# Kernel tuning notes

Measured on AMD Instinct MI355X. Metric: run time of the kernel, lower is better.

Reference implementation:

```python
import jax, jax.numpy as jnp
import numpy as np

LAYER_NAMES = ["self", "cross", "self", "cross", "self", "cross"]
L = len(LAYER_NAMES)
D = 256          # feature_dim
H = 4            # num_heads
HEAD_DIM = D // H
BS = 2           # image pairs
N = 1024         # keypoints per image
BN_EPS = 1e-5


def _conv1x1(x, W, b):
    # x: [B, Cin, N], W: [Cout, Cin] -> [B, Cout, N]  (Conv1d kernel_size=1)
    return jnp.einsum('oi,bin->bon', W, x) + b[None, :, None]


def _batchnorm1d(x, gamma, beta):
    # training-mode BatchNorm1d over [B, C, N]: stats over (B, N) per channel
    mean = jnp.mean(x, axis=(0, 2), keepdims=True)
    var = jnp.var(x, axis=(0, 2), keepdims=True)
    return (x - mean) * jax.lax.rsqrt(var + BN_EPS) * gamma[None, :, None] + beta[None, :, None]


def _attention(q_in, k_in, v_in, mask, Wq, bq, Wk, bk, Wv, bv, Wm, bm):
    B = q_in.shape[0]
    q = _conv1x1(q_in, Wq, bq).reshape(B, HEAD_DIM, H, -1)   # [B, d, h, n]
    k = _conv1x1(k_in, Wk, bk).reshape(B, HEAD_DIM, H, -1)
    v = _conv1x1(v_in, Wv, bv).reshape(B, HEAD_DIM, H, -1)
    scores = jnp.einsum('bdhn,bdhm->bhnm', q, k) / (HEAD_DIM ** 0.5)
    # multiplicative mask (NOT additive), applied before softmax
    scores = scores * mask[:, None, :, :]
    prob = jax.nn.softmax(scores, axis=-1)
    x = jnp.einsum('bhnm,bdhm->bdhn', prob, v)               # [B, d, h, n]
    return _conv1x1(x.reshape(B, D, -1), Wm, bm)             # merge


def _gnn(desc0, desc1, M0, M1, Wq, bq, Wk, bk, Wv, bv, Wm, bm, W1, b1, g1, beta1, W2, b2):
    bs = desc0.shape[0]
    mask = jnp.concatenate([M0, M1], axis=0)                 # [2bs, N, N]
    for i, name in enumerate(LAYER_NAMES):
        x = jnp.concatenate([desc0, desc1], axis=0)          # [2bs, D, N]
        src = jnp.concatenate([desc1, desc0], axis=0) if name == 'cross' else x
        message = _attention(x, src, src, mask,
                             Wq[i], bq[i], Wk[i], bk[i], Wv[i], bv[i], Wm[i], bm[i])
        y = jnp.concatenate([x, message], axis=1)            # [2bs, 2D, N]
        y = jax.nn.relu(_batchnorm1d(_conv1x1(y, W1[i], b1[i]), g1[i], beta1[i]))
        delta = _conv1x1(y, W2[i], b2[i])                    # [2bs, D, N]
        desc0 = desc0 + delta[:bs]
        desc1 = desc1 + delta[bs:]
    # concat the two updated descriptor sets along batch for a single output array
    return jnp.concatenate([desc0, desc1], axis=0)


def setup_inputs() -> dict:
    key = jax.random.key(0)
    ks = jax.random.split(key, 12)
    s = 0.02
    return {
        'desc0': jax.random.normal(ks[0], (BS, D, N), jnp.float32),
        'desc1': jax.random.normal(ks[1], (BS, D, N), jnp.float32),
        'M0': jnp.ones((BS, N, N), jnp.float32),
        'M1': jnp.ones((BS, N, N), jnp.float32),
        'Wq': jax.random.normal(ks[2], (L, D, D), jnp.float32) * s,
        'bq': jnp.zeros((L, D), jnp.float32),
        'Wk': jax.random.normal(ks[3], (L, D, D), jnp.float32) * s,
        'bk': jnp.zeros((L, D), jnp.float32),
        'Wv': jax.random.normal(ks[4], (L, D, D), jnp.float32) * s,
        'bv': jnp.zeros((L, D), jnp.float32),
        'Wm': jax.random.normal(ks[5], (L, D, D), jnp.float32) * s,
        'bm': jnp.zeros((L, D), jnp.float32),
        'W1': jax.random.normal(ks[6], (L, 2 * D, 2 * D), jnp.float32) * s,
        'b1': jnp.zeros((L, 2 * D), jnp.float32),
        'g1': jnp.ones((L, 2 * D), jnp.float32),
        'beta1': jnp.zeros((L, 2 * D), jnp.float32),
        'W2': jax.random.normal(ks[7], (L, D, 2 * D), jnp.float32) * s,
        'b2': jnp.zeros((L, D), jnp.float32),
    }


def reference(desc0, desc1, M0, M1, Wq, bq, Wk, bk, Wv, bv, Wm, bm, W1, b1, g1, beta1, W2, b2):
    return _gnn(desc0, desc1, M0, M1, Wq, bq, Wk, bk, Wv, bv, Wm, bm, W1, b1, g1, beta1, W2, b2)
```

## Files before the change

kernel.cpp:

```cpp
#include <hip/hip_runtime.h>
#include <hip/hip_bf16.h>

#define NN 1024
#define DD 256
#define LL 6

typedef __attribute__((ext_vector_type(8))) short bf16x8;
typedef __attribute__((ext_vector_type(4))) float f32x4;
typedef __attribute__((ext_vector_type(4))) unsigned short u16x4;

__device__ __forceinline__ unsigned short f2bf(float f) {
    union { float f; unsigned u; } x; x.f = f;
    return (unsigned short)((x.u + 0x7fffu + ((x.u >> 16) & 1u)) >> 16);
}

__device__ __forceinline__ unsigned short f2bf_trunc(float f) {
    union { float f; unsigned u; } x; x.f = f;
    return (unsigned short)(x.u >> 16);
}

__device__ __forceinline__ float bf2f(unsigned short u) {
    union { unsigned u; float f; } x; x.u = ((unsigned)u) << 16; return x.f;
}

__device__ __forceinline__ f32x4 mfma16(bf16x8 a, bf16x8 b, f32x4 c) {
    return __builtin_amdgcn_mfma_f32_16x16x32_bf16(a, b, c, 0, 0, 0);
}

__device__ __forceinline__ void gll16(const unsigned short* g, unsigned short* l) {
    __builtin_amdgcn_global_load_lds(
        (const __attribute__((address_space(1))) unsigned int*)g,
        (__attribute__((address_space(3))) unsigned int*)l, 16, 0, 0);
}

__global__ __launch_bounds__(256) void prep_kernel(
    const float* __restrict__ desc0, const float* __restrict__ desc1,
    const float* __restrict__ M0, const float* __restrict__ M1,
    const float* __restrict__ Wq, const float* __restrict__ Wk,
    const float* __restrict__ Wv, const float* __restrict__ Wm,
    const float* __restrict__ W1, const float* __restrict__ W2,
    const float* __restrict__ bm, const float* __restrict__ b1,
    unsigned short* __restrict__ wbf, unsigned short* __restrict__ maskbf,
    float* __restrict__ bmix, float* __restrict__ desc, unsigned short* __restrict__ xbf) {
    __shared__ float T[32][33];
    const int SQ = LL * 65536;
    const int S1 = LL * 262144;
    int blk = blockIdx.x, tid = threadIdx.x;
    if (blk < 3840) {
        int idx = blk * 256 + tid;
        size_t base = (size_t)idx * 4;
        f32x4 v;
        if (base < (size_t)4 * SQ) {
            int seg = (int)(base / SQ), off = (int)(base % SQ);
            const float* p = (seg == 0) ? Wq : (seg == 1) ? Wk : (seg == 2) ? Wv : Wm;
            if (seg < 3) {
                int l = off >> 16, rem = off & 65535;
                int op = rem >> 8, i = rem & 255;
                int src = ((op & 63) << 2) | (op >> 6);
                v = *(const f32x4*)(p + (size_t)l * 65536 + (size_t)src * 256 + i);
            } else {
                v = *(const f32x4*)(p + off);
            }
        } else if (base < (size_t)4 * SQ + S1) {
            v = *(const f32x4*)(W1 + base - 4 * SQ);
        } else {
            v = *(const f32x4*)(W2 + base - 4 * SQ - S1);
        }
        u16x4 o;
#pragma unroll
        for (int j = 0; j < 4; j++) o[j] = f2bf(v[j]);
        *(u16x4*)(wbf + base) = o;
    } else if (blk < 7936) {
        int idx = (blk - 3840) * 256 + tid;
        size_t base = (size_t)idx * 4;
        int bb = (int)(base >> 20);
        const float* src = (bb < 2) ? (M0 + base) : (M1 + base - (2ull << 20));
        f32x4 v = *(const f32x4*)src;
        u16x4 o;
#pragma unroll
        for (int j = 0; j < 4; j++) o[j] = f2bf(v[j]);
        *(u16x4*)(maskbf + base) = o;
    } else if (blk < 8704) {
        int lane = tid & 63;
        int wid = (blk - 7936) * 4 + (tid >> 6);
        int l = wid >> 9, o = wid & 511;
        const float* row = W1 + ((size_t)l * 512 + o) * 512 + 256;
        const float* bmr = bm + (size_t)l * 256;
        f32x4 r = *(const f32x4*)(row + lane * 4);
        f32x4 b4 = *(const f32x4*)(bmr + lane * 4);
        float acc = r[0] * b4[0] + r[1] * b4[1] + r[2] * b4[2] + r[3] * b4[3];
        acc += __shfl_xor(acc, 1, 64);
        acc += __shfl_xor(acc, 2, 64);
        acc += __shfl_xor(acc, 4, 64);
        acc += __shfl_xor(acc, 8, 64);
        acc += __shfl_xor(acc, 16, 64);
        acc += __shfl_xor(acc, 32, 64);
        if (lane == 0) bmix[wid] = b1[wid] + acc;
    } else {
        int task = blk - 8704;
        int bb = task >> 8, tt = task & 255;
        int n0 = (tt >> 3) * 32, c0 = (tt & 7) * 32;
        const float* src = (bb < 2) ? (desc0 + (size_t)bb * DD * NN)
                                    : (desc1 + (size_t)(bb - 2) * DD * NN);
        int i = tid >> 5, j = tid & 31;
#pragma unroll
        for (int r = 0; r < 4; r++) {
            int c = i + r * 8;
            T[c][j] = src[(size_t)(c0 + c) * NN + n0 + j];
        }
        __syncthreads();
#pragma unroll
        for (int r = 0; r < 4; r++) {
            int n = i + r * 8;
            float v = T[j][n];
            size_t di = ((size_t)bb * NN + n0 + n) * DD + c0 + j;
            desc[di] = v;
            xbf[di] = f2bf(v);
        }
    }
}

__global__ __launch_bounds__(256) void fold1_kernel(const unsigned short* __restrict__ W1bf,
                                                    const unsigned short* __restrict__ Wmbf,
                                                    unsigned short* __restrict__ W1m) {
    int l = blockIdx.z;
    int o0 = blockIdx.x * 64, i0 = blockIdx.y * 64;
    const unsigned short* A = W1bf + (size_t)l * 262144;
    const unsigned short* B = Wmbf + (size_t)l * 65536;
    __shared__ unsigned short Bt[64][264];
    int t = threadIdx.x;
#pragma unroll
    for (int r = 0; r < 8; r++) {
        int j = r * 32 + (t >> 3);
        int il = (t & 7) * 8;
        union { bf16x8 v; unsigned short u[8]; } ld;
        ld.v = *(const bf16x8*)(B + (size_t)j * 256 + i0 + il);
#pragma unroll
        for (int jj = 0; jj < 8; jj++) Bt[il + jj][j] = ld.u[jj];
    }
    __syncthreads();
    int w = t >> 6, lane = t & 63, quad = lane >> 4, l15 = lane & 15;
    int wr = (w & 1) * 32, wc = (w >> 1) * 32;
    const unsigned short* Ab = A + (size_t)(o0 + wr + l15) * 512 + 256 + quad * 8;
    f32x4 acc[2][2];
#pragma unroll
    for (int r = 0; r < 2; r++)
#pragma unroll
        for (int c = 0; c < 2; c++) acc[r][c] = (f32x4){0.f, 0.f, 0.f, 0.f};
#pragma unroll
    for (int s = 0; s < 8; s++) {
        int kk = s * 32;
        bf16x8 a0 = *(const bf16x8*)(Ab + kk);
        bf16x8 a1 = *(const bf16x8*)(Ab + 16 * 512 + kk);
        bf16x8 b0 = *(const bf16x8*)(&Bt[wc + l15][kk + quad * 8]);
        bf16x8 b1 = *(const bf16x8*)(&Bt[wc + 16 + l15][kk + quad * 8]);
        acc[0][0] = mfma16(a0, b0, acc[0][0]);
        acc[0][1] = mfma16(a0, b1, acc[0][1]);
        acc[1][0] = mfma16(a1, b0, acc[1][0]);
        acc[1][1] = mfma16(a1, b1, acc[1][1]);
    }
#pragma unroll
    for (int rs = 0; rs < 2; rs++)
#pragma unroll
        for (int cs = 0; cs < 2; cs++)
#pragma unroll
            for (int reg = 0; reg < 4; reg++) {
                int o = o0 + wr + rs * 16 + quad * 4 + reg;
                int i = i0 + wc + cs * 16 + l15;
                int pc = (i & 3) * 64 + (i >> 2);
                W1m[((size_t)l * 512 + o) * 256 + pc] = f2bf(acc[rs][cs][reg]);
            }
}

__global__ __launch_bounds__(256) void final_kernel(const float* __restrict__ desc,
                                                    float* __restrict__ out) {
    __shared__ float T[32][33];
    int bb = blockIdx.z;
    int n0 = blockIdx.x * 32, c0 = blockIdx.y * 32;
    int i = threadIdx.x >> 5, j = threadIdx.x & 31;
#pragma unroll
    for (int r = 0; r < 4; r++) {
        int n = i + r * 8;
        T[n][j] = desc[((size_t)bb * NN + n0 + n) * DD + c0 + j];
    }
    __syncthreads();
#pragma unroll
    for (int r = 0; r < 4; r++) {
        int c = i + r * 8;
        out[((size_t)bb * DD + c0 + c) * NN + n0 + j] = T[j][c];
    }
}

__global__ __launch_bounds__(256) void proj_kernel(
    const unsigned short* __restrict__ xbf,
    const unsigned short* __restrict__ Wq_l, const unsigned short* __restrict__ Wk_l,
    const unsigned short* __restrict__ Wv_l,
    const float* __restrict__ bq_l, const float* __restrict__ bk_l,
    const float* __restrict__ bv_l,
    unsigned short* __restrict__ qb, unsigned short* __restrict__ kb,
    unsigned short* __restrict__ vb, int cross) {
    __shared__ __align__(16) unsigned short sm[8192];
    unsigned short* Al = sm;
    unsigned short* Bl = sm + 4096;

    int m0 = blockIdx.x * 64;
    int by = blockIdx.y;
    int mat = by >> 2;
    int o0c = (by & 3) * 64;
    int bb = m0 >> 10, nloc0 = m0 & 1023;
    int srcbb = (mat == 0) ? bb : (cross ? (bb ^ 2) : bb);
    const unsigned short* A = xbf + (size_t)srcbb * NN * DD + (size_t)nloc0 * DD;
    const unsigned short* W = ((mat == 0) ? Wq_l : (mat == 1) ? Wk_l : Wv_l) + (size_t)o0c * DD;
    const float* bias = (mat == 0) ? bq_l : (mat == 1) ? bk_l : bv_l;

    int tid = threadIdx.x, w = tid >> 6, lane = tid & 63, quad = lane >> 4, l15 = lane & 15;
    int wrow = (w & 1) * 32, wcol = (w >> 1) * 32;
    int lrow = lane >> 3, lcol = (lane & 7) * 8;

    f32x4 acc[2][2];
#pragma unroll
    for (int r = 0; r < 2; r++)
#pragma unroll
        for (int c = 0; c < 2; c++) acc[r][c] = (f32x4){0.f, 0.f, 0.f, 0.f};

    for (int ks = 0; ks < 4; ks++) {
        int k0 = ks * 64;
        __syncthreads();
#pragma unroll
        for (int j = 0; j < 2; j++)
            gll16(A + (size_t)(w * 16 + j * 8 + lrow) * DD + k0 + lcol, Al + (w * 16 + j * 8) * 64);
#pragma unroll
        for (int j = 0; j < 2; j++)
            gll16(W + (size_t)(w * 16 + j * 8 + lrow) * DD + k0 + lcol, Bl + (w * 16 + j * 8) * 64);
        __syncthreads();
#pragma unroll
        for (int kh = 0; kh < 2; kh++) {
            bf16x8 bf[2], af[2];
#pragma unroll
            for (int cs = 0; cs < 2; cs++)
                bf[cs] = *(const bf16x8*)(Bl + (wcol + cs * 16 + l15) * 64 + kh * 32 + quad * 8);
#pragma unroll
            for (int rs = 0; rs < 2; rs++)
                af[rs] = *(const bf16x8*)(Al + (wrow + rs * 16 + l15) * 64 + kh * 32 + quad * 8);
#pragma unroll
            for (int rs = 0; rs < 2; rs++)
#pragma unroll
                for (int cs = 0; cs < 2; cs++)
                    acc[rs][cs] = mfma16(af[rs], bf[cs], acc[rs][cs]);
        }
    }
    __syncthreads();
    float qscale = (mat == 0) ? 0.1803368801f : 1.0f;
    if (mat < 2) {
#pragma unroll
        for (int rs = 0; rs < 2; rs++)
#pragma unroll
            for (int cs = 0; cs < 2; cs++) {
                int op = o0c + wcol + cs * 16 + l15;
                float bv4 = bias[((op & 63) << 2) | (op >> 6)];
#pragma unroll
                for (int reg = 0; reg < 4; reg++)
                    sm[(wrow + rs * 16 + quad * 4 + reg) * 72 + wcol + cs * 16 + l15] =
                        f2bf((acc[rs][cs][reg] + bv4) * qscale);
            }
        __syncthreads();
        int r = tid >> 2, ch = (tid & 3) * 16;
        unsigned short* dst = ((mat == 0) ? qb : kb) + ((size_t)(bb * NN) + nloc0 + r) * 256 + o0c + ch;
        *(bf16x8*)(dst) = *(const bf16x8*)(&sm[r * 72 + ch]);
        *(bf16x8*)(dst + 8) = *(const bf16x8*)(&sm[r * 72 + ch + 8]);
    } else {
#pragma unroll
        for (int rs = 0; rs < 2; rs++)
#pragma unroll
            for (int cs = 0; cs < 2; cs++) {
                int op = o0c + wcol + cs * 16 + l15;
                float bv4 = bias[((op & 63) << 2) | (op >> 6)];
#pragma unroll
                for (int reg = 0; reg < 4; reg++)
                    sm[(wcol + cs * 16 + l15) * 72 + wrow + rs * 16 + quad * 4 + reg] =
                        f2bf(acc[rs][cs][reg] + bv4);
            }
        __syncthreads();
        int o = tid >> 2, nch = (tid & 3) * 16;
        int opg = o0c + o;
        unsigned short* dst = vb + ((size_t)(bb * 4 + (opg >> 6)) * 64 + (opg & 63)) * NN + nloc0 + nch;
        *(bf16x8*)(dst) = *(const bf16x8*)(&sm[o * 72 + nch]);
        *(bf16x8*)(dst + 8) = *(const bf16x8*)(&sm[o * 72 + nch + 8]);
    }
}

__global__ __launch_bounds__(512, 4) void flash_kernel(
    const unsigned short* __restrict__ qb, const unsigned short* __restrict__ kb,
    const unsigned short* __restrict__ vb,
    const unsigned short* __restrict__ maskbf,
    unsigned short* __restrict__ xattn, float* __restrict__ bnsumm) {
    __shared__ __align__(16) char smem[51200];
    unsigned short* Plds = (unsigned short*)smem;
    float* OL = (float*)smem;

    int bh = blockIdx.y, nb = blockIdx.x;
    int bb = bh >> 2, h = bh & 3;
    int tid = threadIdx.x, w = tid >> 6, lane = tid & 63, quad = lane >> 4, l15 = lane & 15;
    int qg = w & 1, sp = w >> 1;

    if (nb == 0 && bh == 0) { bnsumm[tid] = 0.f; bnsumm[tid + 512] = 0.f; }

    const unsigned short* mask = maskbf + (size_t)bb * NN * NN;
    const unsigned short* Q = qb + (size_t)bb * NN * 256 + h * 64;
    const unsigned short* Kb = kb + (size_t)bb * NN * 256 + h * 64;
    const unsigned short* Vb = vb + (size_t)bh * 64 * NN;
    int row0 = nb * 32 + qg * 16;

    bf16x8 qf[2];
#pragma unroll
    for (int kc = 0; kc < 2; kc++)
        qf[kc] = *(const bf16x8*)(Q + (size_t)(row0 + l15) * 256 + kc * 32 + quad * 8);

    const unsigned short* mrow[4];
#pragma unroll
    for (int reg = 0; reg < 4; reg++)
        mrow[reg] = mask + (size_t)(row0 + quad * 4 + reg) * NN + sp * 256;

    f32x4 Oa[4];
#pragma unroll
    for (int dt = 0; dt < 4; dt++) Oa[dt] = (f32x4){0.f, 0.f, 0.f, 0.f};
    float mrun[4], lrun[4];
#pragma unroll
    for (int r = 0; r < 4; r++) { mrun[r] = -1e30f; lrun[r] = 0.f; }

    unsigned short* Pw = Plds + w * (16 * 72);

    for (int mt = 0; mt < 4; mt++) {
        int ml = mt * 64;
        int m0 = sp * 256 + ml;
        f32x4 s4[4];
#pragma unroll
        for (int t = 0; t < 4; t++) s4[t] = (f32x4){0.f, 0.f, 0.f, 0.f};
#pragma unroll
        for (int t = 0; t < 4; t++)
#pragma unroll
            for (int kc = 0; kc < 2; kc++) {
                bf16x8 kf = *(const bf16x8*)(Kb + (size_t)(m0 + t * 16 + l15) * 256 + kc * 32 + quad * 8);
                s4[t] = mfma16(qf[kc], kf, s4[t]);
            }
        bf16x8 vf[8];
#pragma unroll
        for (int dt = 0; dt < 4; dt++)
#pragma unroll
            for (int kc = 0; kc < 2; kc++)
                vf[dt * 2 + kc] = *(const bf16x8*)(Vb + (size_t)(dt * 16 + l15) * NN + m0 + kc * 32 + quad * 8);
        float sv[4][4], rmax[4];
#pragma unroll
        for (int r = 0; r < 4; r++) rmax[r] = -1e30f;
#pragma unroll
        for (int t = 0; t < 4; t++)
#pragma unroll
            for (int reg = 0; reg < 4; reg++) {
                float v = s4[t][reg] * bf2f(mrow[reg][ml + t * 16 + l15]);
                sv[t][reg] = v;
                rmax[reg] = fmaxf(rmax[reg], v);
            }
#pragma unroll
        for (int reg = 0; reg < 4; reg++) {
            rmax[reg] = fmaxf(rmax[reg], __shfl_xor(rmax[reg], 1, 64));
            rmax[reg] = fmaxf(rmax[reg], __shfl_xor(rmax[reg], 2, 64));
            rmax[reg] = fmaxf(rmax[reg], __shfl_xor(rmax[reg], 4, 64));
            rmax[reg] = fmaxf(rmax[reg], __shfl_xor(rmax[reg], 8, 64));
        }
        float alpha[4], rsum[4];
#pragma unroll
        for (int reg = 0; reg < 4; reg++) {
            float mn = fmaxf(mrun[reg], rmax[reg]);
            alpha[reg] = exp2f(mrun[reg] - mn);
            mrun[reg] = mn;
            rsum[reg] = 0.f;
        }
#pragma unroll
        for (int t = 0; t < 4; t++)
#pragma unroll
            for (int reg = 0; reg < 4; reg++) {
                float p = exp2f(sv[t][reg] - mrun[reg]);
                sv[t][reg] = p;
                rsum[reg] += p;
            }
#pragma unroll
        for (int reg = 0; reg < 4; reg++) {
            rsum[reg] += __shfl_xor(rsum[reg], 1, 64);
            rsum[reg] += __shfl_xor(rsum[reg], 2, 64);
            rsum[reg] += __shfl_xor(rsum[reg], 4, 64);
            rsum[reg] += __shfl_xor(rsum[reg], 8, 64);
            lrun[reg] = lrun[reg] * alpha[reg] + rsum[reg];
        }
#pragma unroll
        for (int dt = 0; dt < 4; dt++)
#pragma unroll
            for (int reg = 0; reg < 4; reg++) Oa[dt][reg] *= alpha[reg];
#pragma unroll
        for (int t = 0; t < 4; t++)
#pragma unroll
            for (int reg = 0; reg < 4; reg++)
                Pw[(quad * 4 + reg) * 72 + t * 16 + l15] = f2bf_trunc(sv[t][reg]);
        bf16x8 pf[2];
#pragma unroll
        for (int kc = 0; kc < 2; kc++)
            pf[kc] = *(const bf16x8*)(Pw + l15 * 72 + kc * 32 + quad * 8);
#pragma unroll
        for (int dt = 0; dt < 4; dt++)
#pragma unroll
            for (int kc = 0; kc < 2; kc++)
                Oa[dt] = mfma16(pf[kc], vf[dt * 2 + kc], Oa[dt]);
    }
    __syncthreads();
    float* mine = OL + (size_t)(w * 64 + lane) * 25;
#pragma unroll
    for (int dt = 0; dt < 4; dt++)
#pragma unroll
        for (int reg = 0; reg < 4; reg++) mine[dt * 4 + reg] = Oa[dt][reg];
#pragma unroll
    for (int reg = 0; reg < 4; reg++) { mine[16 + reg] = mrun[reg]; mine[20 + reg] = lrun[reg]; }
    __syncthreads();
    if (sp == 0) {
        const float* p[4];
#pragma unroll
        for (int j = 0; j < 4; j++) p[j] = OL + (size_t)((qg + 2 * j) * 64 + lane) * 25;
        float e[4][4], li[4];
#pragma unroll
        for (int reg = 0; reg < 4; reg++) {
            float M = fmaxf(fmaxf(p[0][16 + reg], p[1][16 + reg]),
                            fmaxf(p[2][16 + reg], p[3][16 + reg]));
            float L = 0.f;
#pragma unroll
            for (int j = 0; j < 4; j++) {
                e[j][reg] = exp2f(p[j][16 + reg] - M);
                L += p[j][20 + reg] * e[j][reg];
            }
            li[reg] = 1.f / L;
        }
#pragma unroll
        for (int dt = 0; dt < 4; dt++)
#pragma unroll
            for (int reg = 0; reg < 4; reg++) {
                float val = 0.f;
#pragma unroll
                for (int j = 0; j < 4; j++) val += p[j][dt * 4 + reg] * e[j][reg];
                val *= li[reg];
                int n = row0 + quad * 4 + reg;
                int col = h * 64 + dt * 16 + l15;
                xattn[((size_t)bb * NN + n) * DD + col] = f2bf(val);
            }
    }
}

__global__ __launch_bounds__(256) void conv1_kernel(
    const unsigned short* __restrict__ xbf, const unsigned short* __restrict__ xattn,
    const unsigned short* __restrict__ W1_l, const unsigned short* __restrict__ W1m_l,
    const float* __restrict__ bmix_l,
    unsigned short* __restrict__ out1, float* __restrict__ bnsumm) {
    __shared__ __align__(16) unsigned short sm[8192];
    unsigned short* Al = sm;
    unsigned short* Bl = sm + 4096;

    int m0 = blockIdx.x * 64, o0 = blockIdx.y * 64;
    int bb = m0 >> 10, nloc0 = m0 & 1023;
    const unsigned short* A1 = xbf + (size_t)bb * NN * DD + (size_t)nloc0 * DD;
    const unsigned short* A2 = xattn + (size_t)bb * NN * DD + (size_t)nloc0 * DD;

    int tid = threadIdx.x, w = tid >> 6, lane = tid & 63, quad = lane >> 4, l15 = lane & 15;
    int wrow = (w & 1) * 32, wcol = (w >> 1) * 32;
    int lrow = lane >> 3, lcol = (lane & 7) * 8;

    f32x4 acc[2][2];
#pragma unroll
    for (int r = 0; r < 2; r++)
#pragma unroll
        for (int c = 0; c < 2; c++) acc[r][c] = (f32x4){0.f, 0.f, 0.f, 0.f};

    for (int ks = 0; ks < 8; ks++) {
        const unsigned short* As = (ks < 4) ? A1 : A2;
        int kloc = (ks & 3) * 64;
        __syncthreads();
#pragma unroll
        for (int j = 0; j < 2; j++)
            gll16(As + (size_t)(w * 16 + j * 8 + lrow) * DD + kloc + lcol, Al + (w * 16 + j * 8) * 64);
#pragma unroll
        for (int j = 0; j < 2; j++) {
            int orow = o0 + w * 16 + j * 8 + lrow;
            const unsigned short* bg = (ks < 4)
                ? (W1_l + (size_t)orow * 512 + ks * 64 + lcol)
                : (W1m_l + (size_t)orow * 256 + (ks - 4) * 64 + lcol);
            gll16(bg, Bl + (w * 16 + j * 8) * 64);
        }
        __syncthreads();
#pragma unroll
        for (int kh = 0; kh < 2; kh++) {
            bf16x8 bf[2], af[2];
#pragma unroll
            for (int cs = 0; cs < 2; cs++)
                bf[cs] = *(const bf16x8*)(Bl + (wcol + cs * 16 + l15) * 64 + kh * 32 + quad * 8);
#pragma unroll
            for (int rs = 0; rs < 2; rs++)
                af[rs] = *(const bf16x8*)(Al + (wrow + rs * 16 + l15) * 64 + kh * 32 + quad * 8);
#pragma unroll
            for (int rs = 0; rs < 2; rs++)
#pragma unroll
                for (int cs = 0; cs < 2; cs++)
                    acc[rs][cs] = mfma16(af[rs], bf[cs], acc[rs][cs]);
        }
    }
    __syncthreads();
    float cs_s[2] = {0.f, 0.f}, cs_q[2] = {0.f, 0.f};
#pragma unroll
    for (int rs = 0; rs < 2; rs++)
#pragma unroll
        for (int cs = 0; cs < 2; cs++) {
            int o = o0 + wcol + cs * 16 + l15;
            float bvx = bmix_l[o];
#pragma unroll
            for (int reg = 0; reg < 4; reg++) {
                float val = acc[rs][cs][reg] + bvx;
                sm[(wrow + rs * 16 + quad * 4 + reg) * 72 + wcol + cs * 16 + l15] = f2bf(val);
                cs_s[cs] += val;
                cs_q[cs] += val * val;
            }
        }
#pragma unroll
    for (int cs = 0; cs < 2; cs++) {
        cs_s[cs] += __shfl_xor(cs_s[cs], 16, 64);
        cs_s[cs] += __shfl_xor(cs_s[cs], 32, 64);
        cs_q[cs] += __shfl_xor(cs_q[cs], 16, 64);
        cs_q[cs] += __shfl_xor(cs_q[cs], 32, 64);
    }
    if (lane < 16) {
#pragma unroll
        for (int cs = 0; cs < 2; cs++) {
            atomicAdd(&bnsumm[o0 + wcol + cs * 16 + lane], cs_s[cs]);
            atomicAdd(&bnsumm[512 + o0 + wcol + cs * 16 + lane], cs_q[cs]);
        }
    }
    __syncthreads();
    int r = tid >> 2, ch = (tid & 3) * 16;
    unsigned short* dst = out1 + ((size_t)(bb * NN) + nloc0 + r) * 512 + o0 + ch;
    *(bf16x8*)(dst) = *(const bf16x8*)(&sm[r * 72 + ch]);
    *(bf16x8*)(dst + 8) = *(const bf16x8*)(&sm[r * 72 + ch + 8]);
}

__global__ __launch_bounds__(256) void bnrelu_kernel(
    const unsigned short* __restrict__ out1, const float* __restrict__ bnsumm,
    const float* __restrict__ g1_l, const float* __restrict__ beta1_l,
    unsigned short* __restrict__ ybf) {
    int idx = blockIdx.x * 256 + threadIdx.x;
    int base = idx * 8;
    int o = base & 511;
    union { bf16x8 v; unsigned short u[8]; } in, op;
    in.v = *(const bf16x8*)(out1 + base);
#pragma unroll
    for (int j = 0; j < 8; j++) {
        int ch = o + j;
        float s = bnsumm[ch], s2 = bnsumm[512 + ch];
        float mean = s * (1.f / 4096.f);
        float var = s2 * (1.f / 4096.f) - mean * mean;
        float sc = g1_l[ch] * rsqrtf(var + 1e-5f);
        float sh = beta1_l[ch] - mean * sc;
        op.u[j] = f2bf(fmaxf(0.f, bf2f(in.u[j]) * sc + sh));
    }
    *(bf16x8*)(ybf + base) = op.v;
}

__global__ __launch_bounds__(256) void conv2_kernel(
    const unsigned short* __restrict__ ybf, const unsigned short* __restrict__ W2_l,
    const float* __restrict__ b2_l, float* __restrict__ desc,
    unsigned short* __restrict__ xbf) {
    __shared__ __align__(16) unsigned short sm[6144];
    unsigned short* Al = sm;
    unsigned short* Bl = sm + 2048;

    int m0 = blockIdx.x * 32, o0 = blockIdx.y * 64;
    int bb = m0 >> 10, nloc0 = m0 & 1023;
    const unsigned short* A = ybf + ((size_t)(bb * NN) + nloc0) * 512;

    int tid = threadIdx.x, w = tid >> 6, lane = tid & 63, quad = lane >> 4, l15 = lane & 15;
    int wr = (w & 1) * 16, wc = (w >> 1) * 32;
    int lrow = lane >> 3, lcol = (lane & 7) * 8;

    f32x4 acc[2];
    acc[0] = (f32x4){0.f, 0.f, 0.f, 0.f};
    acc[1] = (f32x4){0.f, 0.f, 0.f, 0.f};

    for (int ks = 0; ks < 8; ks++) {
        int k0 = ks * 64;
        __syncthreads();
        gll16(A + (size_t)(w * 8 + lrow) * 512 + k0 + lcol, Al + (w * 8) * 64);
#pragma unroll
        for (int j = 0; j < 2; j++)
            gll16(W2_l + (size_t)(o0 + w * 16 + j * 8 + lrow) * 512 + k0 + lcol,
                  Bl + (w * 16 + j * 8) * 64);
        __syncthreads();
#pragma unroll
        for (int kh = 0; kh < 2; kh++) {
            bf16x8 af = *(const bf16x8*)(Al + (wr + l15) * 64 + kh * 32 + quad * 8);
#pragma unroll
            for (int cs = 0; cs < 2; cs++) {
                bf16x8 bf = *(const bf16x8*)(Bl + (wc + cs * 16 + l15) * 64 + kh * 32 + quad * 8);
                acc[cs] = mfma16(af, bf, acc[cs]);
            }
        }
    }
#pragma unroll
    for (int cs = 0; cs < 2; cs++)
#pragma unroll
        for (int reg = 0; reg < 4; reg++) {
            int n = nloc0 + wr + quad * 4 + reg;
            int o = o0 + wc + cs * 16 + l15;
            size_t di = ((size_t)bb * NN + n) * DD + o;
            float nd = desc[di] + acc[cs][reg] + b2_l[o];
            desc[di] = nd;
            xbf[di] = f2bf(nd);
        }
}

extern "C" void kernel_launch(void* const* d_in, const int* in_sizes, int n_in,
                              void* d_out, int out_size, void* d_ws, size_t ws_size,
                              hipStream_t stream) {
    const float* desc0 = (const float*)d_in[0];
    const float* desc1 = (const float*)d_in[1];
    const float* M0p   = (const float*)d_in[2];
    const float* M1p   = (const float*)d_in[3];
    const float* Wq = (const float*)d_in[4];  const float* bq = (const float*)d_in[5];
    const float* Wk = (const float*)d_in[6];  const float* bk = (const float*)d_in[7];
    const float* Wv = (const float*)d_in[8];  const float* bv = (const float*)d_in[9];
    const float* Wm = (const float*)d_in[10]; const float* bm = (const float*)d_in[11];
    const float* W1 = (const float*)d_in[12]; const float* b1 = (const float*)d_in[13];
    const float* g1 = (const float*)d_in[14]; const float* beta1 = (const float*)d_in[15];
    const float* W2 = (const float*)d_in[16]; const float* b2 = (const float*)d_in[17];
    float* out = (float*)d_out;
    char* ws = (char*)d_ws;

    float*          desc   = (float*)(ws);
    unsigned short* xbf    = (unsigned short*)(ws + (4ull << 20));
    unsigned short* qb     = (unsigned short*)(ws + (6ull << 20));
    unsigned short* kbuf   = (unsigned short*)(ws + (8ull << 20));
    unsigned short* vbuf   = (unsigned short*)(ws + (10ull << 20));
    unsigned short* xattn  = (unsigned short*)(ws + (12ull << 20));
    unsigned short* out1   = (unsigned short*)(ws + (14ull << 20));
    float*          bnsumm = (float*)(ws + (18ull << 20));
    float*          bmix   = (float*)(ws + (18ull << 20) + 8192);
    unsigned short* maskbf = (unsigned short*)(ws + (19ull << 20));
    unsigned short* W1m    = (unsigned short*)(ws + (27ull << 20));
    unsigned short* wbf    = (unsigned short*)(ws + (29ull << 20));
    unsigned short* ybf    = (unsigned short*)(ws + (37ull << 20));

    const int SQ = LL * 65536;

    prep_kernel<<<9728, 256, 0, stream>>>(desc0, desc1, M0p, M1p, Wq, Wk, Wv, Wm,
                                          W1, W2, bm, b1, wbf, maskbf, bmix, desc, xbf);
    fold1_kernel<<<dim3(8, 4, 6), 256, 0, stream>>>(wbf + 4 * (size_t)SQ, wbf + 3 * (size_t)SQ, W1m);

    for (int l = 0; l < LL; l++) {
        int cross = l & 1;
        const unsigned short* Wq_l = wbf + (size_t)l * 65536;
        const unsigned short* Wk_l = wbf + SQ + (size_t)l * 65536;
        const unsigned short* Wv_l = wbf + 2 * (size_t)SQ + (size_t)l * 65536;
        const unsigned short* W1_l = wbf + 4 * (size_t)SQ + (size_t)l * 262144;
        const unsigned short* W2_l = wbf + 4 * (size_t)SQ + (size_t)LL * 262144 + (size_t)l * 131072;
        const unsigned short* W1m_l = W1m + (size_t)l * 131072;

        proj_kernel<<<dim3(64, 12), 256, 0, stream>>>(
            xbf, Wq_l, Wk_l, Wv_l, bq + l * 256, bk + l * 256, bv + l * 256,
            qb, kbuf, vbuf, cross);
        flash_kernel<<<dim3(32, 16), 512, 0, stream>>>(qb, kbuf, vbuf, maskbf, xattn, bnsumm);
        conv1_kernel<<<dim3(64, 8), 256, 0, stream>>>(
            xbf, xattn, W1_l, W1m_l, bmix + l * 512, out1, bnsumm);
        bnrelu_kernel<<<1024, 256, 0, stream>>>(out1, bnsumm, g1 + l * 512, beta1 + l * 512, ybf);
        conv2_kernel<<<dim3(128, 4), 256, 0, stream>>>(
            ybf, W2_l, b2 + l * 256, desc, xbf);
    }

    final_kernel<<<dim3(32, 8, 4), 256, 0, stream>>>(desc, out);
}
```

Baseline: 520.8 us.

## Have each flash-attention wave process two query subtiles to reuse K/V fragments

The flash kernel drops from 8 waves to 4 waves per block. Each wave now handles both 16-row query subtiles for its quarter of the keys, so every K and V fragment loaded from global memory feeds two MFMA streams instead of one. This halves K/V global loads per block. In exchange, registers per wave roughly double, fewer threads hide latency, and the softmax work for the two subtiles runs serially within each wave.

```diff
diff --git a/kernel.cpp b/kernel.cpp
--- a/kernel.cpp
+++ b/kernel.cpp
@@ -289,7 +289,7 @@
     }
 }
 
-__global__ __launch_bounds__(512, 4) void flash_kernel(
+__global__ __launch_bounds__(256, 2) void flash_kernel(
     const unsigned short* __restrict__ qb, const unsigned short* __restrict__ kb,
     const unsigned short* __restrict__ vb,
     const unsigned short* __restrict__ maskbf,
@@ -301,47 +301,61 @@
     int bh = blockIdx.y, nb = blockIdx.x;
     int bb = bh >> 2, h = bh & 3;
     int tid = threadIdx.x, w = tid >> 6, lane = tid & 63, quad = lane >> 4, l15 = lane & 15;
-    int qg = w & 1, sp = w >> 1;
-
-    if (nb == 0 && bh == 0) { bnsumm[tid] = 0.f; bnsumm[tid + 512] = 0.f; }
+
+    if (nb == 0 && bh == 0) {
+        bnsumm[tid] = 0.f; bnsumm[tid + 256] = 0.f;
+        bnsumm[tid + 512] = 0.f; bnsumm[tid + 768] = 0.f;
+    }
 
     const unsigned short* mask = maskbf + (size_t)bb * NN * NN;
     const unsigned short* Q = qb + (size_t)bb * NN * 256 + h * 64;
     const unsigned short* Kb = kb + (size_t)bb * NN * 256 + h * 64;
     const unsigned short* Vb = vb + (size_t)bh * 64 * NN;
-    int row0 = nb * 32 + qg * 16;
-
-    bf16x8 qf[2];
-#pragma unroll
-    for (int kc = 0; kc < 2; kc++)
-        qf[kc] = *(const bf16x8*)(Q + (size_t)(row0 + l15) * 256 + kc * 32 + quad * 8);
-
-    const unsigned short* mrow[4];
-#pragma unroll
-    for (int reg = 0; reg < 4; reg++)
-        mrow[reg] = mask + (size_t)(row0 + quad * 4 + reg) * NN + sp * 256;
-
-    f32x4 Oa[4];
-#pragma unroll
-    for (int dt = 0; dt < 4; dt++) Oa[dt] = (f32x4){0.f, 0.f, 0.f, 0.f};
-    float mrun[4], lrun[4];
-#pragma unroll
-    for (int r = 0; r < 4; r++) { mrun[r] = -1e30f; lrun[r] = 0.f; }
+    int row0 = nb * 32;
+
+    bf16x8 qf[2][2];
+#pragma unroll
+    for (int s = 0; s < 2; s++)
+#pragma unroll
+        for (int kc = 0; kc < 2; kc++)
+            qf[s][kc] = *(const bf16x8*)(Q + (size_t)(row0 + s * 16 + l15) * 256 + kc * 32 + quad * 8);
+
+    const unsigned short* mrow[2][4];
+#pragma unroll
+    for (int s = 0; s < 2; s++)
+#pragma unroll
+        for (int reg = 0; reg < 4; reg++)
+            mrow[s][reg] = mask + (size_t)(row0 + s * 16 + quad * 4 + reg) * NN + w * 256;
+
+    f32x4 Oa[2][4];
+#pragma unroll
+    for (int s = 0; s < 2; s++)
+#pragma unroll
+        for (int dt = 0; dt < 4; dt++) Oa[s][dt] = (f32x4){0.f, 0.f, 0.f, 0.f};
+    float mrun[2][4], lrun[2][4];
+#pragma unroll
+    for (int s = 0; s < 2; s++)
+#pragma unroll
+        for (int r = 0; r < 4; r++) { mrun[s][r] = -1e30f; lrun[s][r] = 0.f; }
 
     unsigned short* Pw = Plds + w * (16 * 72);
 
     for (int mt = 0; mt < 4; mt++) {
         int ml = mt * 64;
-        int m0 = sp * 256 + ml;
-        f32x4 s4[4];
-#pragma unroll
-        for (int t = 0; t < 4; t++) s4[t] = (f32x4){0.f, 0.f, 0.f, 0.f};
+        int m0 = w * 256 + ml;
+        f32x4 sA[4], sB[4];
+#pragma unroll
+        for (int t = 0; t < 4; t++) {
+            sA[t] = (f32x4){0.f, 0.f, 0.f, 0.f};
+            sB[t] = (f32x4){0.f, 0.f, 0.f, 0.f};
+        }
 #pragma unroll
         for (int t = 0; t < 4; t++)
 #pragma unroll
             for (int kc = 0; kc < 2; kc++) {
                 bf16x8 kf = *(const bf16x8*)(Kb + (size_t)(m0 + t * 16 + l15) * 256 + kc * 32 + quad * 8);
-                s4[t] = mfma16(qf[kc], kf, s4[t]);
+                sA[t] = mfma16(qf[0][kc], kf, sA[t]);
+                sB[t] = mfma16(qf[1][kc], kf, sB[t]);
             }
         bf16x8 vf[8];
 #pragma unroll
@@ -349,80 +363,87 @@
 #pragma unroll
             for (int kc = 0; kc < 2; kc++)
                 vf[dt * 2 + kc] = *(const bf16x8*)(Vb + (size_t)(dt * 16 + l15) * NN + m0 + kc * 32 + quad * 8);
-        float sv[4][4], rmax[4];
-#pragma unroll
-        for (int r = 0; r < 4; r++) rmax[r] = -1e30f;
-#pragma unroll
-        for (int t = 0; t < 4; t++)
+#pragma unroll
+        for (int s = 0; s < 2; s++) {
+            float sv[4][4], rmax[4];
+#pragma unroll
+            for (int r = 0; r < 4; r++) rmax[r] = -1e30f;
+#pragma unroll
+            for (int t = 0; t < 4; t++)
+#pragma unroll
+                for (int reg = 0; reg < 4; reg++) {
+                    float sc = (s == 0) ? sA[t][reg] : sB[t][reg];
+                    float v = sc * bf2f(mrow[s][reg][ml + t * 16 + l15]);
+                    sv[t][reg] = v;
+                    rmax[reg] = fmaxf(rmax[reg], v);
+                }
 #pragma unroll
             for (int reg = 0; reg < 4; reg++) {
-                float v = s4[t][reg] * bf2f(mrow[reg][ml + t * 16 + l15]);
-                sv[t][reg] = v;
-                rmax[reg] = fmaxf(rmax[reg], v);
-            }
-#pragma unroll
-        for (int reg = 0; reg < 4; reg++) {
-            rmax[reg] = fmaxf(rmax[reg], __shfl_xor(rmax[reg], 1, 64));
-            rmax[reg] = fmaxf(rmax[reg], __shfl_xor(rmax[reg], 2, 64));
-            rmax[reg] = fmaxf(rmax[reg], __shfl_xor(rmax[reg], 4, 64));
-            rmax[reg] = fmaxf(rmax[reg], __shfl_xor(rmax[reg], 8, 64));
-        }
-        float alpha[4], rsum[4];
-#pragma unroll
-        for (int reg = 0; reg < 4; reg++) {
-            float mn = fmaxf(mrun[reg], rmax[reg]);
-            alpha[reg] = exp2f(mrun[reg] - mn);
-            mrun[reg] = mn;
-            rsum[reg] = 0.f;
-        }
-#pragma unroll
-        for (int t = 0; t < 4; t++)
+                rmax[reg] = fmaxf(rmax[reg], __shfl_xor(rmax[reg], 1, 64));
+                rmax[reg] = fmaxf(rmax[reg], __shfl_xor(rmax[reg], 2, 64));
+                rmax[reg] = fmaxf(rmax[reg], __shfl_xor(rmax[reg], 4, 64));
+                rmax[reg] = fmaxf(rmax[reg], __shfl_xor(rmax[reg], 8, 64));
+            }
+            float alpha[4], rsum[4];
 #pragma unroll
             for (int reg = 0; reg < 4; reg++) {
-                float p = exp2f(sv[t][reg] - mrun[reg]);
-                sv[t][reg] = p;
-                rsum[reg] += p;
-            }
-#pragma unroll
-        for (int reg = 0; reg < 4; reg++) {
-            rsum[reg] += __shfl_xor(rsum[reg], 1, 64);
-            rsum[reg] += __shfl_xor(rsum[reg], 2, 64);
-            rsum[reg] += __shfl_xor(rsum[reg], 4, 64);
-            rsum[reg] += __shfl_xor(rsum[reg], 8, 64);
-            lrun[reg] = lrun[reg] * alpha[reg] + rsum[reg];
-        }
+                float mn = fmaxf(mrun[s][reg], rmax[reg]);
+                alpha[reg] = exp2f(mrun[s][reg] - mn);
+                mrun[s][reg] = mn;
+                rsum[reg] = 0.f;
+            }
+#pragma unroll
+            for (int t = 0; t < 4; t++)
+#pragma unroll
+                for (int reg = 0; reg < 4; reg++) {
+                    float p = exp2f(sv[t][reg] - mrun[s][reg]);
+                    sv[t][reg] = p;
+                    rsum[reg] += p;
+                }
+#pragma unroll
+            for (int reg = 0; reg < 4; reg++) {
+                rsum[reg] += __shfl_xor(rsum[reg], 1, 64);
+                rsum[reg] += __shfl_xor(rsum[reg], 2, 64);
+                rsum[reg] += __shfl_xor(rsum[reg], 4, 64);
+                rsum[reg] += __shfl_xor(rsum[reg], 8, 64);
+                lrun[s][reg] = lrun[s][reg] * alpha[reg] + rsum[reg];
+            }
+#pragma unroll
+            for (int dt = 0; dt < 4; dt++)
+#pragma unroll
+                for (int reg = 0; reg < 4; reg++) Oa[s][dt][reg] *= alpha[reg];
+#pragma unroll
+            for (int t = 0; t < 4; t++)
+#pragma unroll
+                for (int reg = 0; reg < 4; reg++)
+                    Pw[(quad * 4 + reg) * 72 + t * 16 + l15] = f2bf_trunc(sv[t][reg]);
+            bf16x8 pf[2];
+#pragma unroll
+            for (int kc = 0; kc < 2; kc++)
+                pf[kc] = *(const bf16x8*)(Pw + l15 * 72 + kc * 32 + quad * 8);
+#pragma unroll
+            for (int dt = 0; dt < 4; dt++)
+#pragma unroll
+                for (int kc = 0; kc < 2; kc++)
+                    Oa[s][dt] = mfma16(pf[kc], vf[dt * 2 + kc], Oa[s][dt]);
+        }
+    }
+    __syncthreads();
+#pragma unroll
+    for (int s = 0; s < 2; s++) {
+        float* mine = OL + (size_t)((s + 2 * w) * 64 + lane) * 25;
 #pragma unroll
         for (int dt = 0; dt < 4; dt++)
 #pragma unroll
-            for (int reg = 0; reg < 4; reg++) Oa[dt][reg] *= alpha[reg];
-#pragma unroll
-        for (int t = 0; t < 4; t++)
-#pragma unroll
-            for (int reg = 0; reg < 4; reg++)
-                Pw[(quad * 4 + reg) * 72 + t * 16 + l15] = f2bf_trunc(sv[t][reg]);
-        bf16x8 pf[2];
-#pragma unroll
-        for (int kc = 0; kc < 2; kc++)
-            pf[kc] = *(const bf16x8*)(Pw + l15 * 72 + kc * 32 + quad * 8);
-#pragma unroll
-        for (int dt = 0; dt < 4; dt++)
-#pragma unroll
-            for (int kc = 0; kc < 2; kc++)
-                Oa[dt] = mfma16(pf[kc], vf[dt * 2 + kc], Oa[dt]);
+            for (int reg = 0; reg < 4; reg++) mine[dt * 4 + reg] = Oa[s][dt][reg];
+#pragma unroll
+        for (int reg = 0; reg < 4; reg++) { mine[16 + reg] = mrun[s][reg]; mine[20 + reg] = lrun[s][reg]; }
     }
     __syncthreads();
-    float* mine = OL + (size_t)(w * 64 + lane) * 25;
-#pragma unroll
-    for (int dt = 0; dt < 4; dt++)
-#pragma unroll
-        for (int reg = 0; reg < 4; reg++) mine[dt * 4 + reg] = Oa[dt][reg];
-#pragma unroll
-    for (int reg = 0; reg < 4; reg++) { mine[16 + reg] = mrun[reg]; mine[20 + reg] = lrun[reg]; }
-    __syncthreads();
-    if (sp == 0) {
+    if (w < 2) {
         const float* p[4];
 #pragma unroll
-        for (int j = 0; j < 4; j++) p[j] = OL + (size_t)((qg + 2 * j) * 64 + lane) * 25;
+        for (int j = 0; j < 4; j++) p[j] = OL + (size_t)((w + 2 * j) * 64 + lane) * 25;
         float e[4][4], li[4];
 #pragma unroll
         for (int reg = 0; reg < 4; reg++) {
@@ -444,7 +465,7 @@
 #pragma unroll
                 for (int j = 0; j < 4; j++) val += p[j][dt * 4 + reg] * e[j][reg];
                 val *= li[reg];
-                int n = row0 + quad * 4 + reg;
+                int n = row0 + w * 16 + quad * 4 + reg;
                 int col = h * 64 + dt * 16 + l15;
                 xattn[((size_t)bb * NN + n) * DD + col] = f2bf(val);
             }
@@ -667,7 +688,7 @@
         proj_kernel<<<dim3(64, 12), 256, 0, stream>>>(
             xbf, Wq_l, Wk_l, Wv_l, bq + l * 256, bk + l * 256, bv + l * 256,
             qb, kbuf, vbuf, cross);
-        flash_kernel<<<dim3(32, 16), 512, 0, stream>>>(qb, kbuf, vbuf, maskbf, xattn, bnsumm);
+        flash_kernel<<<dim3(32, 16), 256, 0, stream>>>(qb, kbuf, vbuf, maskbf, xattn, bnsumm);
         conv1_kernel<<<dim3(64, 8), 256, 0, stream>>>(
             xbf, xattn, W1_l, W1m_l, bmix + l * 512, out1, bnsumm);
         bnrelu_kernel<<<1024, 256, 0, stream>>>(out1, bnsumm, g1 + l * 512, beta1 + l * 512, ybf);
```

Measured after the change: 465.8 us. 10.6% less time.
